# Optimization experiments

Hardware: AMD Instinct MI355X
Metric: run time of the kernel (lower is better)

## Reference

```python
import jax, jax.numpy as jnp
import numpy as np

N_NODES = 100000
N_EDGES = 1000000
D_IN = 64
FEATURES = [64, 64, 16]


def setup_inputs() -> dict:
    key = jax.random.key(0)
    ks = jax.random.split(key, 10)
    nodes = jax.random.normal(ks[0], (N_NODES, D_IN), dtype=jnp.float32)
    senders = jax.random.randint(ks[1], (N_EDGES,), 0, N_NODES, dtype=jnp.int64)
    receivers = jax.random.randint(ks[2], (N_EDGES,), 0, N_NODES, dtype=jnp.int64)
    dims = [D_IN] + FEATURES
    params = {}
    for i in range(len(FEATURES)):
        fan_in = dims[i]
        # hk.Linear default: truncated-normal-ish init; plain normal scaled is fine for a reference
        params[f"W{i}"] = jax.random.normal(ks[3 + i], (dims[i], dims[i + 1]), dtype=jnp.float32) / np.sqrt(fan_in)
        params[f"b{i}"] = jnp.zeros((dims[i + 1],), dtype=jnp.float32)
    return {"nodes": nodes, "senders": senders, "receivers": receivers, **params}


def _gcn_layer(h, senders, receivers, W, b, use_tanh, add_self_edges):
    N = h.shape[0]
    h = h @ W + b
    if use_tanh:
        h = jnp.tanh(h)
    if add_self_edges:
        self_idx = jnp.arange(N, dtype=senders.dtype)
        s = jnp.concatenate([senders, self_idx], axis=0)
        r = jnp.concatenate([receivers, self_idx], axis=0)
    else:
        s, r = senders, receivers
    ones = jnp.ones(s.shape, dtype=h.dtype)
    deg_s = jax.ops.segment_sum(ones, s, num_segments=N)
    deg_r = jax.ops.segment_sum(ones, r, num_segments=N)
    h = h * jax.lax.rsqrt(jnp.maximum(deg_s, 1.0))[:, None]
    h = jax.ops.segment_sum(h[s], r, num_segments=N)  # gather -> scatter-add
    h = h * jax.lax.rsqrt(jnp.maximum(deg_r, 1.0))[:, None]
    return h


def reference(nodes, senders, receivers, W0, b0, W1, b1, W2, b2):
    h = nodes
    # layers over features[:-1]: tanh activation, self edges added
    h = _gcn_layer(h, senders, receivers, W0, b0, use_tanh=True, add_self_edges=True)
    h = _gcn_layer(h, senders, receivers, W1, b1, use_tanh=True, add_self_edges=True)
    # final layer: linear only, no self edges, still symmetric normalization
    h = _gcn_layer(h, senders, receivers, W2, b2, use_tanh=False, add_self_edges=False)
    return h
```

## Files before the change

kernel.cpp:

```cpp
#include <hip/hip_runtime.h>


#define CAP 32
#define BSH 7
#define BW 128
#define BCAP 1664
#define EPT 16

typedef unsigned short u16;
typedef unsigned int u32;

__device__ __forceinline__ float bf2f(u16 u) {
    return __uint_as_float(((u32)u) << 16);
}
__device__ __forceinline__ u16 f2bf(float f) {
    u32 x = __float_as_uint(f);
    u32 r = x + 0x7fff + ((x >> 16) & 1);
    return (u16)(r >> 16);
}
__device__ __forceinline__ float fast_tanh(float x) {
    x = fminf(15.f, fmaxf(-15.f, x));
    float e = __expf(2.f * x);
    return (e - 1.f) / (e + 1.f);
}
__device__ __forceinline__ int unpack_deg(const u32* pk, int n) {
    return (int)((pk[n >> 2] >> (8 * (n & 3))) & 255u);
}

__global__ __launch_bounds__(256) void k_init(int* __restrict__ curR,
                                              int* __restrict__ curS, int nbuk) {
    int t = blockIdx.x * 256 + threadIdx.x;
    if (t < nbuk) {
        curR[t] = t * BCAP;
        curS[t] = t * BCAP;
    }
}

__global__ __launch_bounds__(1024) void k_part(const int* __restrict__ s,
                                               const int* __restrict__ r,
                                               int* __restrict__ curR,
                                               int* __restrict__ curS,
                                               int2* __restrict__ pairR,
                                               int* __restrict__ svalS,
                                               int E, int nbuk) {
    __shared__ int cR[1024], cS[1024], bR[1024], bS[1024];
    const int t = threadIdx.x;
    for (int i = t; i < nbuk; i += 1024) { cR[i] = 0; cS[i] = 0; }
    __syncthreads();

    int ss[EPT], rr[EPT];
    const int base = blockIdx.x * (1024 * EPT);
#pragma unroll
    for (int i = 0; i < EPT; ++i) {
        int e = base + i * 1024 + t;
        ss[i] = (e < E) ? s[e] : -1;
        rr[i] = (e < E) ? r[e] : -1;
    }
#pragma unroll
    for (int i = 0; i < EPT; ++i) {
        if (rr[i] >= 0) {
            atomicAdd(&cR[rr[i] >> BSH], 1);
            atomicAdd(&cS[ss[i] >> BSH], 1);
        }
    }
    __syncthreads();
    for (int i = t; i < nbuk; i += 1024) {
        bR[i] = cR[i] ? atomicAdd(&curR[i], cR[i]) : 0;
        bS[i] = cS[i] ? atomicAdd(&curS[i], cS[i]) : 0;
    }
    __syncthreads();
    for (int i = t; i < nbuk; i += 1024) { cR[i] = 0; cS[i] = 0; }
    __syncthreads();
#pragma unroll
    for (int i = 0; i < EPT; ++i) {
        if (rr[i] >= 0) {
            int rb = rr[i] >> BSH;
            int pos = bR[rb] + atomicAdd(&cR[rb], 1);
            if (pos < (rb + 1) * BCAP) pairR[pos] = make_int2(ss[i], rr[i]);
            int sb = ss[i] >> BSH;
            int ps = bS[sb] + atomicAdd(&cS[sb], 1);
            if (ps < (sb + 1) * BCAP) svalS[ps] = ss[i];
        }
    }
}

__global__ __launch_bounds__(256) void k_ellb(const int2* __restrict__ pairR,
                                              const int* __restrict__ curR,
                                              int* __restrict__ ell,
                                              u32* __restrict__ degIp) {
    __shared__ int degLoc[BW];
    const int b = blockIdx.x, t = threadIdx.x;
    if (t < BW) degLoc[t] = 0;
    __syncthreads();
    const int start = b * BCAP;
    const int cnt = min(curR[b] - start, BCAP);
    for (int e = t; e < cnt; e += 256) {
        int2 p = pairR[start + e];
        int slot = atomicAdd(&degLoc[p.y - (b << BSH)], 1);
        if (slot < CAP) ell[p.y * CAP + slot] = p.x;
    }
    __syncthreads();
    if (t < BW / 4) {
        u32 w = (u32)min(degLoc[4 * t], 255) |
                ((u32)min(degLoc[4 * t + 1], 255) << 8) |
                ((u32)min(degLoc[4 * t + 2], 255) << 16) |
                ((u32)min(degLoc[4 * t + 3], 255) << 24);
        degIp[(b << (BSH - 2)) + t] = w;
    }
}

__global__ __launch_bounds__(256) void k_dego(const int* __restrict__ svalS,
                                              const int* __restrict__ curS,
                                              u32* __restrict__ degOp) {
    __shared__ int degLoc[BW];
    const int b = blockIdx.x, t = threadIdx.x;
    if (t < BW) degLoc[t] = 0;
    __syncthreads();
    const int start = b * BCAP;
    const int cnt = min(curS[b] - start, BCAP);
    for (int e = t; e < cnt; e += 256) {
        atomicAdd(&degLoc[svalS[start + e] - (b << BSH)], 1);
    }
    __syncthreads();
    if (t < BW / 4) {
        u32 w = (u32)min(degLoc[4 * t], 255) |
                ((u32)min(degLoc[4 * t + 1], 255) << 8) |
                ((u32)min(degLoc[4 * t + 2], 255) << 16) |
                ((u32)min(degLoc[4 * t + 3], 255) << 24);
        degOp[(b << (BSH - 2)) + t] = w;
    }
}

__global__ __launch_bounds__(256) void k_transform64(const float* __restrict__ in,
                                                     const float* __restrict__ W,
                                                     const float* __restrict__ b,
                                                     const u32* __restrict__ degOp,
                                                     u16* __restrict__ out, int N) {
    __shared__ float4 lds[4][128];
    const int lane = threadIdx.x & 63;
    const int wv = threadIdx.x >> 6;

    float wc[64];
#pragma unroll
    for (int k = 0; k < 64; ++k) wc[k] = W[k * 64 + lane];
    const float bias = b[lane];

    const int base = blockIdx.x * 32 + wv * 8;
    const float4* in4 = (const float4*)in;
#pragma unroll
    for (int r2 = 0; r2 < 2; ++r2) {
        int idx = r2 * 64 + lane;
        int nn = base + (idx >> 4);
        float4 v = {0.f, 0.f, 0.f, 0.f};
        if (nn < N) v = in4[(size_t)base * 16 + idx];
        lds[wv][idx] = v;
    }
#pragma unroll
    for (int i = 0; i < 8; ++i) {
        const int n = base + i;
        if (n >= N) break;
        float acc = 0.f;
#pragma unroll
        for (int kk = 0; kk < 16; ++kk) {
            float4 h = lds[wv][i * 16 + kk];
            acc = fmaf(h.x, wc[4 * kk + 0], acc);
            acc = fmaf(h.y, wc[4 * kk + 1], acc);
            acc = fmaf(h.z, wc[4 * kk + 2], acc);
            acc = fmaf(h.w, wc[4 * kk + 3], acc);
        }
        float as01 = rsqrtf((float)unpack_deg(degOp, n) + 1.f);
        acc = fast_tanh(acc + bias) * as01;
        out[(size_t)n * 64 + lane] = f2bf(acc);
    }
}

__global__ __launch_bounds__(256) void k_fgt64(const u16* __restrict__ h,
                                               const u32* __restrict__ degOp,
                                               const u32* __restrict__ degIp,
                                               const int* __restrict__ ell,
                                               const float* __restrict__ W,
                                               const float* __restrict__ b,
                                               u16* __restrict__ y, int N) {
    __shared__ float4 lds[4][16];
    const int lane = threadIdx.x & 63;
    const int wv = threadIdx.x >> 6;
    const int g = lane >> 4, c = lane & 15;

    float wc[64];
#pragma unroll
    for (int k = 0; k < 64; ++k) wc[k] = W[k * 64 + lane];
    const float bias = b[lane];

    const ushort4* h4 = (const ushort4*)h;
    const int base = blockIdx.x * 32 + wv * 8;
    for (int i8 = 0; i8 < 8; ++i8) {
        const int n = base + i8;
        if (n >= N) break;
        const int di = unpack_deg(degIp, n);
        const int deg = min(di, CAP);
        int idxv = (lane < CAP) ? ell[n * CAP + lane] : 0;

        float4 acc = {0.f, 0.f, 0.f, 0.f};
        const int jn = (deg + 3) >> 2;
        for (int j = 0; j < jn; ++j) {
            int i = g + 4 * j;
            int id = __shfl(idxv, i, 64);
            if (i < deg) {
                ushort4 v = h4[(size_t)id * 16 + c];
                acc.x += bf2f(v.x); acc.y += bf2f(v.y);
                acc.z += bf2f(v.z); acc.w += bf2f(v.w);
            }
        }
#pragma unroll
        for (int m = 16; m <= 32; m <<= 1) {
            acc.x += __shfl_xor(acc.x, m, 64);
            acc.y += __shfl_xor(acc.y, m, 64);
            acc.z += __shfl_xor(acc.z, m, 64);
            acc.w += __shfl_xor(acc.w, m, 64);
        }
        ushort4 sv = h4[(size_t)n * 16 + c];
        acc.x += bf2f(sv.x); acc.y += bf2f(sv.y);
        acc.z += bf2f(sv.z); acc.w += bf2f(sv.w);
        if (g == 0) lds[wv][c] = acc;

        const float inscale = rsqrtf((float)di + 1.f);
        const float outscale = rsqrtf((float)unpack_deg(degOp, n) + 1.f);
        float dot = 0.f;
        const float* row = (const float*)lds[wv];
#pragma unroll
        for (int k = 0; k < 64; k += 4) {
            float4 hh = *(const float4*)(row + k);
            dot = fmaf(hh.x, wc[k + 0], dot);
            dot = fmaf(hh.y, wc[k + 1], dot);
            dot = fmaf(hh.z, wc[k + 2], dot);
            dot = fmaf(hh.w, wc[k + 3], dot);
        }
        float v = fast_tanh(fmaf(dot, inscale, bias)) * outscale;
        y[(size_t)n * 64 + lane] = f2bf(v);
    }
}

__global__ __launch_bounds__(256) void k_fgt16(const u16* __restrict__ h,
                                               const u32* __restrict__ degOp,
                                               const u32* __restrict__ degIp,
                                               const int* __restrict__ ell,
                                               const float* __restrict__ W,
                                               const float* __restrict__ b,
                                               u16* __restrict__ y16, int N) {
    __shared__ float4 lds[4][16];
    const int lane = threadIdx.x & 63;
    const int wv = threadIdx.x >> 6;
    const int g = lane >> 4, c = lane & 15;
    const int j = lane & 15;

    float wc[16];
#pragma unroll
    for (int kk = 0; kk < 16; ++kk) wc[kk] = W[(16 * g + kk) * 16 + j];
    const float bias = b[j];

    const ushort4* h4 = (const ushort4*)h;
    const int base = blockIdx.x * 32 + wv * 8;
    for (int i8 = 0; i8 < 8; ++i8) {
        const int n = base + i8;
        if (n >= N) break;
        const int di = unpack_deg(degIp, n);
        const int deg = min(di, CAP);
        int idxv = (lane < CAP) ? ell[n * CAP + lane] : 0;

        float4 acc = {0.f, 0.f, 0.f, 0.f};
        const int jn = (deg + 3) >> 2;
        for (int jj = 0; jj < jn; ++jj) {
            int i = g + 4 * jj;
            int id = __shfl(idxv, i, 64);
            if (i < deg) {
                ushort4 v = h4[(size_t)id * 16 + c];
                acc.x += bf2f(v.x); acc.y += bf2f(v.y);
                acc.z += bf2f(v.z); acc.w += bf2f(v.w);
            }
        }
#pragma unroll
        for (int m = 16; m <= 32; m <<= 1) {
            acc.x += __shfl_xor(acc.x, m, 64);
            acc.y += __shfl_xor(acc.y, m, 64);
            acc.z += __shfl_xor(acc.z, m, 64);
            acc.w += __shfl_xor(acc.w, m, 64);
        }
        ushort4 sv = h4[(size_t)n * 16 + c];
        acc.x += bf2f(sv.x); acc.y += bf2f(sv.y);
        acc.z += bf2f(sv.z); acc.w += bf2f(sv.w);
        if (g == 0) lds[wv][c] = acc;

        const float* row = (const float*)lds[wv];
        float dot = 0.f;
#pragma unroll
        for (int kk = 0; kk < 16; ++kk) dot = fmaf(row[16 * g + kk], wc[kk], dot);
#pragma unroll
        for (int m = 16; m <= 32; m <<= 1) dot += __shfl_xor(dot, m, 64);

        if (g == 0) {
            const float inscale = rsqrtf((float)di + 1.f);
            const float outscale = rsqrtf(fmaxf((float)unpack_deg(degOp, n), 1.f));
            float v = fmaf(dot, inscale, bias) * outscale;
            y16[(size_t)n * 16 + j] = f2bf(v);
        }
    }
}

__global__ __launch_bounds__(256) void k_g16(const u16* __restrict__ h,
                                             const u32* __restrict__ degIp,
                                             const int* __restrict__ ell,
                                             float* __restrict__ out, int N) {
    const int lane = threadIdx.x & 63;
    const int wv = threadIdx.x >> 6;
    const int n = blockIdx.x * 4 + wv;
    if (n >= N) return;
    const int g = lane >> 2, c = lane & 3;
    const int di = unpack_deg(degIp, n);
    const int deg = min(di, CAP);
    int idxv = (lane < CAP) ? ell[n * CAP + lane] : 0;

    const ushort4* h4 = (const ushort4*)h;
    float4 acc = {0.f, 0.f, 0.f, 0.f};
    const int jn = (deg + 15) >> 4;
    for (int j = 0; j < jn; ++j) {
        int i = g + 16 * j;
        int id = __shfl(idxv, i, 64);
        if (i < deg) {
            ushort4 v = h4[(size_t)id * 4 + c];
            acc.x += bf2f(v.x); acc.y += bf2f(v.y);
            acc.z += bf2f(v.z); acc.w += bf2f(v.w);
        }
    }
#pragma unroll
    for (int m = 4; m <= 32; m <<= 1) {
        acc.x += __shfl_xor(acc.x, m, 64);
        acc.y += __shfl_xor(acc.y, m, 64);
        acc.z += __shfl_xor(acc.z, m, 64);
        acc.w += __shfl_xor(acc.w, m, 64);
    }
    if (g == 0) {
        float sc = rsqrtf(fmaxf((float)di, 1.f));
        acc.x *= sc; acc.y *= sc; acc.z *= sc; acc.w *= sc;
        ((float4*)out)[(size_t)n * 4 + c] = acc;
    }
}

extern "C" void kernel_launch(void* const* d_in, const int* in_sizes, int n_in,
                              void* d_out, int out_size, void* d_ws, size_t ws_size,
                              hipStream_t stream) {
    const float* nodes = (const float*)d_in[0];
    const int* senders = (const int*)d_in[1];
    const int* receivers = (const int*)d_in[2];
    const float* W0 = (const float*)d_in[3];
    const float* b0 = (const float*)d_in[4];
    const float* W1 = (const float*)d_in[5];
    const float* b1 = (const float*)d_in[6];
    const float* W2 = (const float*)d_in[7];
    const float* b2 = (const float*)d_in[8];
    float* out = (float*)d_out;

    const int N = in_sizes[0] / 64;
    const int E = in_sizes[1];
    const int nbuk = (N + BW - 1) >> BSH;
    const int nwords = nbuk * (BW / 4);

    u16* A = (u16*)d_ws;
    u16* B = A + (size_t)N * 64;
    u16* Y16 = B + (size_t)N * 64;
    u32* degOp = (u32*)(Y16 + (size_t)N * 16);
    u32* degIp = degOp + nwords;
    int* curR = (int*)(degIp + nwords);
    int* curS = curR + nbuk;
    int* ell = (int*)(curS + nbuk);
    int2* pairR = (int2*)(ell + (size_t)N * CAP);
    int* svalS = (int*)(pairR + (size_t)nbuk * BCAP);

    k_init<<<(nbuk + 255) / 256, 256, 0, stream>>>(curR, curS, nbuk);
    const int pblk = (E + 1024 * EPT - 1) / (1024 * EPT);
    k_part<<<pblk, 1024, 0, stream>>>(senders, receivers, curR, curS,
                                      pairR, svalS, E, nbuk);
    k_ellb<<<nbuk, 256, 0, stream>>>(pairR, curR, ell, degIp);
    k_dego<<<nbuk, 256, 0, stream>>>(svalS, curS, degOp);

    const int tb = (N + 31) / 32;
    const int fb = (N + 31) / 32;
    const int gb = (N + 3) / 4;

    k_transform64<<<tb, 256, 0, stream>>>(nodes, W0, b0, degOp, A, N);
    k_fgt64<<<fb, 256, 0, stream>>>(A, degOp, degIp, ell, W1, b1, B, N);
    k_fgt16<<<fb, 256, 0, stream>>>(B, degOp, degIp, ell, W2, b2, Y16, N);
    k_g16<<<gb, 256, 0, stream>>>(Y16, degIp, ell, out, N);
}
```

Measured before the change: 272.4 us.

## Apply 64-to-16 projection before layer-2 aggregation to gather narrow rows

The second layer's linear map is linear, so W2 is now applied to each node's 64-wide features first, in a new transform kernel that writes 16-wide bf16 rows. The aggregation then gathers 16-wide neighbour rows instead of 64-wide ones, which cuts gather traffic by about four times at the cost of an extra kernel launch and an intermediate buffer. The k_g16 kernel is also rewritten to process 8 nodes per wave with a fixed two-iteration unrolled gather loop, and bf16 rounding of the projected values adds a small precision change.

```diff
diff --git a/kernel.cpp b/kernel.cpp
--- a/kernel.cpp
+++ b/kernel.cpp
@@ -240,14 +240,9 @@
     }
 }
 
-__global__ __launch_bounds__(256) void k_fgt16(const u16* __restrict__ h,
-                                               const u32* __restrict__ degOp,
-                                               const u32* __restrict__ degIp,
-                                               const int* __restrict__ ell,
-                                               const float* __restrict__ W,
-                                               const float* __restrict__ b,
-                                               u16* __restrict__ y16, int N) {
-    __shared__ float4 lds[4][16];
+__global__ __launch_bounds__(256) void k_t16(const u16* __restrict__ h,
+                                             const float* __restrict__ W,
+                                             u16* __restrict__ c16, int N) {
     const int lane = threadIdx.x & 63;
     const int wv = threadIdx.x >> 6;
     const int g = lane >> 4, c = lane & 15;
@@ -256,8 +251,95 @@
     float wc[16];
 #pragma unroll
     for (int kk = 0; kk < 16; ++kk) wc[kk] = W[(16 * g + kk) * 16 + j];
-    const float bias = b[j];
-
+
+    const ushort4* h4 = (const ushort4*)h;
+    const int base = blockIdx.x * 32 + wv * 8;
+    for (int i8 = 0; i8 < 8; ++i8) {
+        const int n = base + i8;
+        if (n >= N) break;
+        ushort4 sv = h4[(size_t)n * 16 + c];
+        float4 a = {bf2f(sv.x), bf2f(sv.y), bf2f(sv.z), bf2f(sv.w)};
+        float dot = 0.f;
+#pragma unroll
+        for (int q = 0; q < 4; ++q) {
+            int src = 4 * g + q;
+            float hx = __shfl(a.x, src, 64);
+            float hy = __shfl(a.y, src, 64);
+            float hz = __shfl(a.z, src, 64);
+            float hw = __shfl(a.w, src, 64);
+            dot = fmaf(hx, wc[4 * q + 0], dot);
+            dot = fmaf(hy, wc[4 * q + 1], dot);
+            dot = fmaf(hz, wc[4 * q + 2], dot);
+            dot = fmaf(hw, wc[4 * q + 3], dot);
+        }
+        dot += __shfl_xor(dot, 16, 64);
+        dot += __shfl_xor(dot, 32, 64);
+        if (g == 0) c16[(size_t)n * 16 + j] = f2bf(dot);
+    }
+}
+
+__global__ __launch_bounds__(256) void k_fg16(const u16* __restrict__ c16in,
+                                              const u32* __restrict__ degOp,
+                                              const u32* __restrict__ degIp,
+                                              const int* __restrict__ ell,
+                                              const float* __restrict__ b2,
+                                              u16* __restrict__ y16, int N) {
+    const int lane = threadIdx.x & 63;
+    const int wv = threadIdx.x >> 6;
+    const int g = lane >> 2, c = lane & 3;
+    const float4 b2v = ((const float4*)b2)[c];
+
+    const ushort4* h4 = (const ushort4*)c16in;
+    const int base = blockIdx.x * 32 + wv * 8;
+    for (int i8 = 0; i8 < 8; ++i8) {
+        const int n = base + i8;
+        if (n >= N) break;
+        const int di = unpack_deg(degIp, n);
+        const int deg = min(di, CAP);
+        int idxv = (lane < CAP) ? ell[n * CAP + lane] : 0;
+
+        float4 acc = {0.f, 0.f, 0.f, 0.f};
+#pragma unroll
+        for (int j = 0; j < 2; ++j) {
+            int i = g + 16 * j;
+            int id = __shfl(idxv, i, 64);
+            if (i < deg) {
+                ushort4 v = h4[(size_t)id * 4 + c];
+                acc.x += bf2f(v.x); acc.y += bf2f(v.y);
+                acc.z += bf2f(v.z); acc.w += bf2f(v.w);
+            }
+        }
+#pragma unroll
+        for (int m = 4; m <= 32; m <<= 1) {
+            acc.x += __shfl_xor(acc.x, m, 64);
+            acc.y += __shfl_xor(acc.y, m, 64);
+            acc.z += __shfl_xor(acc.z, m, 64);
+            acc.w += __shfl_xor(acc.w, m, 64);
+        }
+        ushort4 sv = h4[(size_t)n * 4 + c];
+        acc.x += bf2f(sv.x); acc.y += bf2f(sv.y);
+        acc.z += bf2f(sv.z); acc.w += bf2f(sv.w);
+
+        if (g == 0) {
+            const float inscale = rsqrtf((float)di + 1.f);
+            const float outscale = rsqrtf(fmaxf((float)unpack_deg(degOp, n), 1.f));
+            ushort4 o;
+            o.x = f2bf(fmaf(acc.x, inscale, b2v.x) * outscale);
+            o.y = f2bf(fmaf(acc.y, inscale, b2v.y) * outscale);
+            o.z = f2bf(fmaf(acc.z, inscale, b2v.z) * outscale);
+            o.w = f2bf(fmaf(acc.w, inscale, b2v.w) * outscale);
+            ((ushort4*)y16)[(size_t)n * 4 + c] = o;
+        }
+    }
+}
+
+__global__ __launch_bounds__(256) void k_g16(const u16* __restrict__ h,
+                                             const u32* __restrict__ degIp,
+                                             const int* __restrict__ ell,
+                                             float* __restrict__ out, int N) {
+    const int lane = threadIdx.x & 63;
+    const int wv = threadIdx.x >> 6;
+    const int g = lane >> 2, c = lane & 3;
     const ushort4* h4 = (const ushort4*)h;
     const int base = blockIdx.x * 32 + wv * 8;
     for (int i8 = 0; i8 < 8; ++i8) {
@@ -268,80 +350,28 @@
         int idxv = (lane < CAP) ? ell[n * CAP + lane] : 0;
 
         float4 acc = {0.f, 0.f, 0.f, 0.f};
-        const int jn = (deg + 3) >> 2;
-        for (int jj = 0; jj < jn; ++jj) {
-            int i = g + 4 * jj;
+#pragma unroll
+        for (int j = 0; j < 2; ++j) {
+            int i = g + 16 * j;
             int id = __shfl(idxv, i, 64);
             if (i < deg) {
-                ushort4 v = h4[(size_t)id * 16 + c];
+                ushort4 v = h4[(size_t)id * 4 + c];
                 acc.x += bf2f(v.x); acc.y += bf2f(v.y);
                 acc.z += bf2f(v.z); acc.w += bf2f(v.w);
             }
         }
 #pragma unroll
-        for (int m = 16; m <= 32; m <<= 1) {
+        for (int m = 4; m <= 32; m <<= 1) {
             acc.x += __shfl_xor(acc.x, m, 64);
             acc.y += __shfl_xor(acc.y, m, 64);
             acc.z += __shfl_xor(acc.z, m, 64);
             acc.w += __shfl_xor(acc.w, m, 64);
         }
-        ushort4 sv = h4[(size_t)n * 16 + c];
-        acc.x += bf2f(sv.x); acc.y += bf2f(sv.y);
-        acc.z += bf2f(sv.z); acc.w += bf2f(sv.w);
-        if (g == 0) lds[wv][c] = acc;
-
-        const float* row = (const float*)lds[wv];
-        float dot = 0.f;
-#pragma unroll
-        for (int kk = 0; kk < 16; ++kk) dot = fmaf(row[16 * g + kk], wc[kk], dot);
-#pragma unroll
-        for (int m = 16; m <= 32; m <<= 1) dot += __shfl_xor(dot, m, 64);
-
         if (g == 0) {
-            const float inscale = rsqrtf((float)di + 1.f);
-            const float outscale = rsqrtf(fmaxf((float)unpack_deg(degOp, n), 1.f));
-            float v = fmaf(dot, inscale, bias) * outscale;
-            y16[(size_t)n * 16 + j] = f2bf(v);
-        }
-    }
-}
-
-__global__ __launch_bounds__(256) void k_g16(const u16* __restrict__ h,
-                                             const u32* __restrict__ degIp,
-                                             const int* __restrict__ ell,
-                                             float* __restrict__ out, int N) {
-    const int lane = threadIdx.x & 63;
-    const int wv = threadIdx.x >> 6;
-    const int n = blockIdx.x * 4 + wv;
-    if (n >= N) return;
-    const int g = lane >> 2, c = lane & 3;
-    const int di = unpack_deg(degIp, n);
-    const int deg = min(di, CAP);
-    int idxv = (lane < CAP) ? ell[n * CAP + lane] : 0;
-
-    const ushort4* h4 = (const ushort4*)h;
-    float4 acc = {0.f, 0.f, 0.f, 0.f};
-    const int jn = (deg + 15) >> 4;
-    for (int j = 0; j < jn; ++j) {
-        int i = g + 16 * j;
-        int id = __shfl(idxv, i, 64);
-        if (i < deg) {
-            ushort4 v = h4[(size_t)id * 4 + c];
-            acc.x += bf2f(v.x); acc.y += bf2f(v.y);
-            acc.z += bf2f(v.z); acc.w += bf2f(v.w);
-        }
-    }
-#pragma unroll
-    for (int m = 4; m <= 32; m <<= 1) {
-        acc.x += __shfl_xor(acc.x, m, 64);
-        acc.y += __shfl_xor(acc.y, m, 64);
-        acc.z += __shfl_xor(acc.z, m, 64);
-        acc.w += __shfl_xor(acc.w, m, 64);
-    }
-    if (g == 0) {
-        float sc = rsqrtf(fmaxf((float)di, 1.f));
-        acc.x *= sc; acc.y *= sc; acc.z *= sc; acc.w *= sc;
-        ((float4*)out)[(size_t)n * 4 + c] = acc;
+            float sc = rsqrtf(fmaxf((float)di, 1.f));
+            acc.x *= sc; acc.y *= sc; acc.z *= sc; acc.w *= sc;
+            ((float4*)out)[(size_t)n * 4 + c] = acc;
+        }
     }
 }
 
@@ -367,7 +397,8 @@
     u16* A = (u16*)d_ws;
     u16* B = A + (size_t)N * 64;
     u16* Y16 = B + (size_t)N * 64;
-    u32* degOp = (u32*)(Y16 + (size_t)N * 16);
+    u16* C16 = Y16 + (size_t)N * 16;
+    u32* degOp = (u32*)(C16 + (size_t)N * 16);
     u32* degIp = degOp + nwords;
     int* curR = (int*)(degIp + nwords);
     int* curS = curR + nbuk;
@@ -382,12 +413,11 @@
     k_ellb<<<nbuk, 256, 0, stream>>>(pairR, curR, ell, degIp);
     k_dego<<<nbuk, 256, 0, stream>>>(svalS, curS, degOp);
 
-    const int tb = (N + 31) / 32;
     const int fb = (N + 31) / 32;
-    const int gb = (N + 3) / 4;
-
-    k_transform64<<<tb, 256, 0, stream>>>(nodes, W0, b0, degOp, A, N);
+
+    k_transform64<<<fb, 256, 0, stream>>>(nodes, W0, b0, degOp, A, N);
     k_fgt64<<<fb, 256, 0, stream>>>(A, degOp, degIp, ell, W1, b1, B, N);
-    k_fgt16<<<fb, 256, 0, stream>>>(B, degOp, degIp, ell, W2, b2, Y16, N);
-    k_g16<<<gb, 256, 0, stream>>>(Y16, degIp, ell, out, N);
-}
+    k_t16<<<fb, 256, 0, stream>>>(B, W2, C16, N);
+    k_fg16<<<fb, 256, 0, stream>>>(C16, degOp, degIp, ell, b2, Y16, N);
+    k_g16<<<fb, 256, 0, stream>>>(Y16, degIp, ell, out, N);
+}
```

After: 280.0 us. 2.8% more time.
